# Optimization experiments

Measured on AMD Instinct MI355X. Metric: run time of the kernel, lower is better.

## Reference

```python
import jax, jax.numpy as jnp
import numpy as np
from jax import lax

B, T, C_IN = 64, 1000, 12
D_MODEL, D_STATE, D_CONV, EXPAND = 128, 16, 4, 2
D_INNER = EXPAND * D_MODEL          # 256
DT_RANK = (D_MODEL + 15) // 16      # ceil(d_model/16) = 8
NUM_CLASSES = 5


def setup_inputs() -> dict:
    key = jax.random.key(0)
    ks = jax.random.split(key, 12)
    s = 0.05
    f = jnp.float32
    return {
        "x": jax.random.normal(ks[0], (B, T, C_IN), f),
        # input projection Linear(C_IN, D_MODEL) with bias
        "ip_w": jax.random.normal(ks[1], (D_MODEL, C_IN), f) * s,
        "ip_b": jnp.zeros((D_MODEL,), f),
        # Mamba block params (mamba_ssm layout)
        "in_proj_w": jax.random.normal(ks[2], (2 * D_INNER, D_MODEL), f) * s,
        "conv_w": jax.random.normal(ks[3], (D_INNER, D_CONV), f) * s,
        "conv_b": jnp.zeros((D_INNER,), f),
        "x_proj_w": jax.random.normal(ks[4], (DT_RANK + 2 * D_STATE, D_INNER), f) * s,
        "dt_proj_w": jax.random.normal(ks[5], (D_INNER, DT_RANK), f) * s,
        "dt_proj_b": jax.random.uniform(ks[6], (D_INNER,), f, -4.0, -2.0),  # softplus -> small positive dt
        "A_log": jnp.log(jnp.tile(jnp.arange(1, D_STATE + 1, dtype=f), (D_INNER, 1))),
        "D_skip": jnp.ones((D_INNER,), f),
        "out_proj_w": jax.random.normal(ks[7], (D_MODEL, D_INNER), f) * s,
        # classifier head: Linear(128,64) -> ReLU -> Linear(64,5)
        "fc1_w": jax.random.normal(ks[8], (64, D_MODEL), f) * s,
        "fc1_b": jnp.zeros((64,), f),
        "fc2_w": jax.random.normal(ks[9], (NUM_CLASSES, 64), f) * s,
        "fc2_b": jnp.zeros((NUM_CLASSES,), f),
    }


def _silu(x):
    return x * jax.nn.sigmoid(x)


def _mamba(h, in_proj_w, conv_w, conv_b, x_proj_w, dt_proj_w, dt_proj_b,
           A_log, D_skip, out_proj_w):
    # h: (B, T, D_MODEL)
    xz = h @ in_proj_w.T                              # (B, T, 2*Di)
    xm, z = jnp.split(xz, 2, axis=-1)
    # depthwise causal conv over time (pad left d_conv-1)
    xp = jnp.pad(xm, ((0, 0), (D_CONV - 1, 0), (0, 0)))
    rhs = conv_w.T[:, None, :]                        # (d_conv, 1, Di)
    xc = lax.conv_general_dilated(
        xp, rhs, (1,), 'VALID',
        dimension_numbers=('NHC', 'HIO', 'NHC'),
        feature_group_count=D_INNER) + conv_b
    u = _silu(xc)                                     # (B, T, Di)
    dbc = u @ x_proj_w.T                              # (B, T, dt_rank + 2N)
    dt = dbc[..., :DT_RANK]
    Bm = dbc[..., DT_RANK:DT_RANK + D_STATE]          # (B, T, N)
    Cm = dbc[..., DT_RANK + D_STATE:]                 # (B, T, N)
    delta = jax.nn.softplus(dt @ dt_proj_w.T + dt_proj_b)  # (B, T, Di)
    A = -jnp.exp(A_log)                               # (Di, N)

    def step(hst, inp):
        d_t, b_t, c_t, u_t = inp                      # (B,Di),(B,N),(B,N),(B,Di)
        dA = jnp.exp(d_t[..., None] * A)              # (B, Di, N)
        hst = dA * hst + (d_t * u_t)[..., None] * b_t[:, None, :]
        y_t = jnp.einsum('bdn,bn->bd', hst, c_t)
        return hst, y_t

    h0 = jnp.zeros((h.shape[0], D_INNER, D_STATE), h.dtype)
    _, ys = lax.scan(step, h0, (delta.transpose(1, 0, 2), Bm.transpose(1, 0, 2),
                                Cm.transpose(1, 0, 2), u.transpose(1, 0, 2)))
    y = ys.transpose(1, 0, 2) + u * D_skip            # (B, T, Di)
    y = y * _silu(z)
    return y @ out_proj_w.T                           # (B, T, D_MODEL)


def reference(x, ip_w, ip_b, in_proj_w, conv_w, conv_b, x_proj_w, dt_proj_w,
              dt_proj_b, A_log, D_skip, out_proj_w, fc1_w, fc1_b, fc2_w, fc2_b):
    h = x @ ip_w.T + ip_b                             # (B, T, D_MODEL)
    y = _mamba(h, in_proj_w, conv_w, conv_b, x_proj_w, dt_proj_w, dt_proj_b,
               A_log, D_skip, out_proj_w)
    last = y[:, -1, :]                                # (B, D_MODEL)
    hid = jax.nn.relu(last @ fc1_w.T + fc1_b)
    return hid @ fc2_w.T + fc2_b                      # (B, NUM_CLASSES)
```

## Files before the change

kernel.cpp:

```cpp
#include <hip/hip_runtime.h>
#include <cstddef>

#define T_LEN 1000
#define B_SZ 64
#define C_IN_ 12
#define D_MODEL_ 128
#define D_INNER_ 256
#define D_STATE_ 16
#define DT_RANK_ 8
#define N_CLS 5
#define NCH 5

typedef __attribute__((ext_vector_type(8))) short bf16x8;
typedef __attribute__((ext_vector_type(8))) unsigned short u16x8;
typedef __attribute__((ext_vector_type(4))) float f32x4;

__device__ __forceinline__ float fast_exp2(float x) {
#if __has_builtin(__builtin_amdgcn_exp2f)
  return __builtin_amdgcn_exp2f(x);
#else
  float r; asm volatile("v_exp_f32 %0, %1" : "=v"(r) : "v"(x)); return r;
#endif
}
__device__ __forceinline__ float fast_log2(float x) {
#if __has_builtin(__builtin_amdgcn_logf)
  return __builtin_amdgcn_logf(x);
#else
  float r; asm volatile("v_log_f32 %0, %1" : "=v"(r) : "v"(x)); return r;
#endif
}
__device__ __forceinline__ float fast_rcp(float x) {
#if __has_builtin(__builtin_amdgcn_rcpf)
  return __builtin_amdgcn_rcpf(x);
#else
  float r; asm volatile("v_rcp_f32 %0, %1" : "=v"(r) : "v"(x)); return r;
#endif
}
__device__ __forceinline__ float silu_f(float x) {
  float den = 1.f + fast_exp2(-x * 1.4426950408889634f);
  return x * fast_rcp(den);
}
__device__ __forceinline__ float softplus_f(float x) {
  const float L = 1.4426950408889634f, iL = 0.6931471805599453f;
  float e = fast_exp2(-fabsf(x) * L);
  float l = fast_log2(1.f + e) * iL;
  return fmaxf(x, 0.f) + l;
}
__device__ __forceinline__ unsigned short f2bf(float f) {
  unsigned u = __builtin_bit_cast(unsigned, f);
  u = u + 0x7FFFu + ((u >> 16) & 1u);
  return (unsigned short)(u >> 16);
}
__device__ __forceinline__ float bf2f(unsigned short h) {
  unsigned u = ((unsigned)h) << 16;
  return __builtin_bit_cast(float, u);
}

__global__ __launch_bounds__(256) void k0_prep(
    const float* __restrict__ x, const float* __restrict__ ip_w,
    const float* __restrict__ ip_b, const float* __restrict__ in_proj_w,
    char* __restrict__ h_pk, char* __restrict__ w_pk)
{
  __shared__ unsigned short pk_s[8192];
  __shared__ unsigned short pkw_s[32768];
  const int tid = threadIdx.x;

  if (blockIdx.x == 16) {
    if (blockIdx.y != 0) return;
    const int n = tid;
    for (int k = 0; k < D_MODEL_; ++k) {
      unsigned short v = f2bf(in_proj_w[(size_t)n * D_MODEL_ + k]);
      int off = ((n >> 4) * 4 + (k >> 5)) * 512 + ((k & 31) >> 3) * 128
              + (n & 15) * 8 + (k & 7);
      pkw_s[off] = v;
    }
    __syncthreads();
    const float4* s4 = (const float4*)pkw_s;
    float4* dst = (float4*)w_pk;
#pragma unroll
    for (int q = 0; q < 16; ++q) dst[tid * 16 + q] = s4[tid * 16 + q];
    return;
  }

  const int tile4 = blockIdx.x;
  const int b = blockIdx.y;
  const int rl = tid & 63;
  const int kc = (tid >> 6) * 32;
  const int t = tile4 * 64 + rl;

  float xr[C_IN_] = {0.f, 0.f, 0.f, 0.f, 0.f, 0.f, 0.f, 0.f, 0.f, 0.f, 0.f, 0.f};
  const bool valid = (t < T_LEN);
  if (valid) {
    const float4* xp = (const float4*)(x + ((size_t)b * T_LEN + t) * C_IN_);
    float4 v0 = xp[0], v1 = xp[1], v2 = xp[2];
    xr[0] = v0.x; xr[1] = v0.y; xr[2] = v0.z;  xr[3] = v0.w;
    xr[4] = v1.x; xr[5] = v1.y; xr[6] = v1.z;  xr[7] = v1.w;
    xr[8] = v2.x; xr[9] = v2.y; xr[10] = v2.z; xr[11] = v2.w;
  }
  for (int kk = 0; kk < 32; ++kk) {
    const int k = kc + kk;
    unsigned short v = 0;
    if (valid) {
      float acc = ip_b[k];
      const float* wr = ip_w + k * C_IN_;
#pragma unroll
      for (int c = 0; c < C_IN_; ++c) acc += xr[c] * wr[c];
      v = f2bf(acc);
    }
    int off = (rl >> 4) * 2048 + (k >> 5) * 512 + ((k & 31) >> 3) * 128
            + (rl & 15) * 8 + (k & 7);
    pk_s[off] = v;
  }
  __syncthreads();
  const float4* s4 = (const float4*)pk_s;
  float4* dst = (float4*)(h_pk + (size_t)(b * 64 + tile4 * 4) * 4096);
#pragma unroll
  for (int q = 0; q < 4; ++q) dst[tid * 4 + q] = s4[tid * 4 + q];
}

__global__ __launch_bounds__(256) void k1_u(
    const char* __restrict__ h_pk, const char* __restrict__ w_pk,
    const float* __restrict__ conv_w, const float* __restrict__ conv_b,
    float* __restrict__ u_out)
{
  __shared__ float xm[67][260];

  const int tile = blockIdx.x;
  const int b    = blockIdx.y;
  const int t0   = tile * 64;
  const int tid  = threadIdx.x;
  const int w    = tid >> 6;
  const int l    = tid & 63;

  {
    const char* achunk = h_pk + (size_t)(b * 64 + tile * 4 + w) * 4096;
    bf16x8 a0 = *(const bf16x8*)(achunk + 0 * 1024 + l * 16);
    bf16x8 a1 = *(const bf16x8*)(achunk + 1 * 1024 + l * 16);
    bf16x8 a2 = *(const bf16x8*)(achunk + 2 * 1024 + l * 16);
    bf16x8 a3 = *(const bf16x8*)(achunk + 3 * 1024 + l * 16);

    const int row_l = w * 16 + (l >> 4) * 4;
#pragma unroll
    for (int nt = 0; nt < 16; ++nt) {
      const char* wb = w_pk + (size_t)nt * 4096 + l * 16;
      bf16x8 b0 = *(const bf16x8*)(wb + 0 * 1024);
      bf16x8 b1 = *(const bf16x8*)(wb + 1 * 1024);
      bf16x8 b2 = *(const bf16x8*)(wb + 2 * 1024);
      bf16x8 b3 = *(const bf16x8*)(wb + 3 * 1024);
      f32x4 acc = {0.f, 0.f, 0.f, 0.f};
      acc = __builtin_amdgcn_mfma_f32_16x16x32_bf16(a0, b0, acc, 0, 0, 0);
      acc = __builtin_amdgcn_mfma_f32_16x16x32_bf16(a1, b1, acc, 0, 0, 0);
      acc = __builtin_amdgcn_mfma_f32_16x16x32_bf16(a2, b2, acc, 0, 0, 0);
      acc = __builtin_amdgcn_mfma_f32_16x16x32_bf16(a3, b3, acc, 0, 0, 0);
      const int col = nt * 16 + (l & 15);
#pragma unroll
      for (int r = 0; r < 4; ++r)
        xm[3 + row_l + r][col] = acc[r];
    }
  }

  {
    const int n = tid;
    float hac[3] = {0.f, 0.f, 0.f};
    if (tile > 0) {
      const char* wrow = w_pk + (size_t)(n >> 4) * 4096 + (n & 15) * 16;
#pragma unroll
      for (int kt = 0; kt < 4; ++kt)
#pragma unroll
        for (int lg = 0; lg < 4; ++lg) {
          u16x8 wv = *(const u16x8*)(wrow + kt * 1024 + lg * 256);
#pragma unroll
          for (int r = 0; r < 3; ++r) {
            const int t = t0 - 3 + r;
            const char* hc = h_pk + (size_t)(b * 64 + (t >> 4)) * 4096;
            u16x8 hv = *(const u16x8*)(hc + kt * 1024 + lg * 256 + (t & 15) * 16);
#pragma unroll
            for (int j = 0; j < 8; ++j) hac[r] += bf2f(hv[j]) * bf2f(wv[j]);
          }
        }
    }
#pragma unroll
    for (int r = 0; r < 3; ++r) xm[r][n] = hac[r];
  }
  __syncthreads();

  {
    const int n = tid;
    const float4 cw = *(const float4*)&conv_w[n * 4];
    const float  cb = conv_b[n];
    float x0 = xm[0][n], x1 = xm[1][n], x2 = xm[2][n];
    for (int i = 0; i < 64; ++i) {
      const int t = t0 + i;
      float x3 = xm[3 + i][n];
      if (t < T_LEN) {
        float s = cb + x0 * cw.x + x1 * cw.y + x2 * cw.z + x3 * cw.w;
        u_out[(((size_t)b * T_LEN + t) << 8) + n] = silu_f(s);
      }
      x0 = x1; x1 = x2; x2 = x3;
    }
  }
}

__global__ __launch_bounds__(256) void k3_delta(
    const float* __restrict__ u, const float* __restrict__ x_proj_w,
    const float* __restrict__ dt_proj_w, const float* __restrict__ dt_proj_b,
    float* __restrict__ delta_T, float* __restrict__ du_T,
    float* __restrict__ pk_bm, float* __restrict__ u_last)
{
  __shared__ float4 xp4[24][65];
  __shared__ float dt_s[64][9];
  __shared__ float bm_s[64][17];

  const int row0 = blockIdx.x * 64;
  const int tid = threadIdx.x;

  for (int f = tid; f < 24 * 64; f += 256) {
    int c = f >> 6, k4 = f & 63;
    xp4[c][k4] = *(const float4*)&x_proj_w[(size_t)c * 256 + k4 * 4];
  }
  const float4 w0 = *(const float4*)&dt_proj_w[(size_t)tid * 8];
  const float4 w1 = *(const float4*)&dt_proj_w[(size_t)tid * 8 + 4];
  const float bias = dt_proj_b[tid];
  __syncthreads();

  {
    const int r2 = tid >> 3, cg = tid & 7;
    const int ra = 2 * r2;
    const float4* ua4 = (const float4*)(u + (size_t)(row0 + ra) * 256);
    const float4* ub4 = (const float4*)(u + (size_t)(row0 + ra + 1) * 256);
    float a0 = 0.f, a1 = 0.f, a2 = 0.f, b0 = 0.f, b1 = 0.f, b2 = 0.f;
    for (int k4 = 0; k4 < 64; ++k4) {
      float4 a = ua4[k4], bb = ub4[k4];
      float4 q0 = xp4[cg * 3 + 0][k4];
      float4 q1 = xp4[cg * 3 + 1][k4];
      float4 q2 = xp4[cg * 3 + 2][k4];
      a0 += a.x * q0.x + a.y * q0.y + a.z * q0.z + a.w * q0.w;
      a1 += a.x * q1.x + a.y * q1.y + a.z * q1.z + a.w * q1.w;
      a2 += a.x * q2.x + a.y * q2.y + a.z * q2.z + a.w * q2.w;
      b0 += bb.x * q0.x + bb.y * q0.y + bb.z * q0.z + bb.w * q0.w;
      b1 += bb.x * q1.x + bb.y * q1.y + bb.z * q1.z + bb.w * q1.w;
      b2 += bb.x * q2.x + bb.y * q2.y + bb.z * q2.z + bb.w * q2.w;
    }
    float va[2][3] = {{a0, a1, a2}, {b0, b1, b2}};
#pragma unroll
    for (int rr = 0; rr < 2; ++rr)
#pragma unroll
      for (int c = 0; c < 3; ++c) {
        int col = cg * 3 + c;
        int row = ra + rr;
        if (col < 8) dt_s[row][col] = va[rr][c];
        else bm_s[row][col - 8] = va[rr][c];
      }
  }
  __syncthreads();

  for (int g = 0; g < 8; ++g) {
    float dd[8], uu[8];
#pragma unroll
    for (int j = 0; j < 8; ++j) {
      int r = g * 8 + j;
      float pre = bias
        + dt_s[r][0] * w0.x + dt_s[r][1] * w0.y + dt_s[r][2] * w0.z + dt_s[r][3] * w0.w
        + dt_s[r][4] * w1.x + dt_s[r][5] * w1.y + dt_s[r][6] * w1.z + dt_s[r][7] * w1.w;
      float dlt = softplus_f(pre);
      size_t o = (size_t)(row0 + r) * 256 + tid;
      float uv = u[o];
      dd[j] = dlt;
      uu[j] = dlt * uv;
      int rowg = row0 + r;
      if ((rowg - (rowg / 1000) * 1000) == 999)
        u_last[(rowg / 1000) * 256 + tid] = uv;
    }
    int row = row0 + g * 8;
    int bb_ = row / 1000;
    int t   = row - bb_ * 1000;
    size_t rb = ((size_t)(bb_ * 256 + tid)) * 1000 + t;
    *(float4*)&delta_T[rb]     = make_float4(dd[0], dd[1], dd[2], dd[3]);
    *(float4*)&delta_T[rb + 4] = make_float4(dd[4], dd[5], dd[6], dd[7]);
    *(float4*)&du_T[rb]        = make_float4(uu[0], uu[1], uu[2], uu[3]);
    *(float4*)&du_T[rb + 4]    = make_float4(uu[4], uu[5], uu[6], uu[7]);
  }
  if (tid < 16) {
    for (int g = 0; g < 8; ++g) {
      float pb[8];
#pragma unroll
      for (int j = 0; j < 8; ++j) pb[j] = bm_s[g * 8 + j][tid];
      int row = row0 + g * 8;
      int bb_ = row / 1000;
      int t   = row - bb_ * 1000;
      size_t base = (((size_t)bb_ * 250 + (t >> 2)) * 16 + tid) * 4;
      *(float4*)&pk_bm[base]      = make_float4(pb[0], pb[1], pb[2], pb[3]);
      *(float4*)&pk_bm[base + 64] = make_float4(pb[4], pb[5], pb[6], pb[7]);
    }
  }
}

__global__ __launch_bounds__(256) void k4_scan(
    const float* __restrict__ delta_T, const float* __restrict__ du_T,
    const float* __restrict__ pk_bm, const float* __restrict__ A_log,
    float* __restrict__ Qb, float* __restrict__ Pb)
{
  __shared__ float bs[50][16][4];

  const int d0 = blockIdx.x * 16;
  const int b  = blockIdx.y;
  const int c  = blockIdx.z;
  const int tid = threadIdx.x;
  const int dl = tid >> 4;
  const int n  = tid & 15;
  const int d  = d0 + dl;

  {
    const float4* src = (const float4*)(pk_bm + ((size_t)b * 250 + (size_t)c * 50) * 64);
    float4* dst = (float4*)bs;
    for (int f = tid; f < 800; f += 256) dst[f] = src[f];
  }
  const float A2 = -expf(A_log[(size_t)d * 16 + n]) * 1.4426950408889634f;
  const float* dp = delta_T + ((size_t)(b * 256 + d)) * 1000 + c * 200;
  const float* xp = du_T    + ((size_t)(b * 256 + d)) * 1000 + c * 200;
  __syncthreads();

  float s = 0.f, sum = 0.f;
#pragma unroll
  for (int i = 0; i < 50; ++i) {
    float4 dv = *(const float4*)(dp + 4 * i);
    float4 xv = *(const float4*)(xp + 4 * i);
    float4 bv = *(const float4*)&bs[i][n][0];
    sum += (dv.x + dv.y) + (dv.z + dv.w);
    s = fast_exp2(dv.x * A2) * s + xv.x * bv.x;
    s = fast_exp2(dv.y * A2) * s + xv.y * bv.y;
    s = fast_exp2(dv.z * A2) * s + xv.z * bv.z;
    s = fast_exp2(dv.w * A2) * s + xv.w * bv.w;
  }

  const size_t o = (size_t)c * 262144 + (size_t)b * 4096 + (size_t)d0 * 16 + tid;
  Qb[o] = s;
  Pb[o] = fast_exp2(A2 * sum);
}

__global__ __launch_bounds__(256) void k4b_combine(
    const float* __restrict__ Qb, const float* __restrict__ Pb,
    float* __restrict__ state_out)
{
  const size_t g = (size_t)blockIdx.x * 256 + threadIdx.x;
  float s = Qb[g];
#pragma unroll
  for (int c = 1; c < NCH; ++c)
    s = Qb[(size_t)c * 262144 + g] + Pb[(size_t)c * 262144 + g] * s;
  state_out[g] = s;
}

__global__ __launch_bounds__(256) void k5_head(
    const float* __restrict__ x, const float* __restrict__ ip_w,
    const float* __restrict__ ip_b, const float* __restrict__ in_proj_w,
    const float* __restrict__ x_proj_w, const float* __restrict__ u_last,
    const float* __restrict__ state, const float* __restrict__ D_skip,
    const float* __restrict__ out_proj_w, const float* __restrict__ fc1_w,
    const float* __restrict__ fc1_b, const float* __restrict__ fc2_w,
    const float* __restrict__ fc2_b, float* __restrict__ out)
{
  const int b = blockIdx.x, tid = threadIdx.x;
  __shared__ float hl[128], ul[256], zs[256], cm[16], yv[256], ov[128], hid[64];
  if (tid < 128) {
    float acc = ip_b[tid];
    const float* xr = x + ((size_t)b * T_LEN + (T_LEN - 1)) * C_IN_;
#pragma unroll
    for (int c = 0; c < C_IN_; ++c) acc += xr[c] * ip_w[tid * C_IN_ + c];
    hl[tid] = acc;
  }
  ul[tid] = u_last[b * 256 + tid];
  __syncthreads();
  {
    float acc = 0.f;
    const float4* wv = (const float4*)(in_proj_w + (size_t)(256 + tid) * 128);
    const float4* h4 = (const float4*)hl;
    for (int k = 0; k < 32; ++k) {
      float4 a = wv[k], c = h4[k];
      acc += c.x * a.x + c.y * a.y + c.z * a.z + c.w * a.w;
    }
    zs[tid] = silu_f(acc);
  }
  if (tid < 16) {
    float acc = 0.f;
    const float4* wv = (const float4*)(x_proj_w + (size_t)(24 + tid) * 256);
    const float4* u4 = (const float4*)ul;
    for (int k = 0; k < 64; ++k) {
      float4 a = wv[k], c = u4[k];
      acc += c.x * a.x + c.y * a.y + c.z * a.z + c.w * a.w;
    }
    cm[tid] = acc;
  }
  __syncthreads();
  {
    const float* st = state + ((size_t)b * 256 + tid) * 16;
    float acc = 0.f;
#pragma unroll
    for (int n = 0; n < 16; ++n) acc += st[n] * cm[n];
    yv[tid] = (acc + ul[tid] * D_skip[tid]) * zs[tid];
  }
  __syncthreads();
  if (tid < 128) {
    float acc = 0.f;
    const float4* wv = (const float4*)(out_proj_w + (size_t)tid * 256);
    const float4* y4 = (const float4*)yv;
    for (int k = 0; k < 64; ++k) {
      float4 a = wv[k], c = y4[k];
      acc += c.x * a.x + c.y * a.y + c.z * a.z + c.w * a.w;
    }
    ov[tid] = acc;
  }
  __syncthreads();
  if (tid < 64) {
    float acc = fc1_b[tid];
    const float4* wv = (const float4*)(fc1_w + (size_t)tid * 128);
    const float4* o4 = (const float4*)ov;
    for (int k = 0; k < 32; ++k) {
      float4 a = wv[k], c = o4[k];
      acc += c.x * a.x + c.y * a.y + c.z * a.z + c.w * a.w;
    }
    hid[tid] = fmaxf(acc, 0.f);
  }
  __syncthreads();
  if (tid < N_CLS) {
    float acc = fc2_b[tid];
    const float* wv = fc2_w + (size_t)tid * 64;
    for (int k = 0; k < 64; ++k) acc += hid[k] * wv[k];
    out[b * N_CLS + tid] = acc;
  }
}

extern "C" void kernel_launch(void* const* d_in, const int* in_sizes, int n_in,
                              void* d_out, int out_size, void* d_ws, size_t ws_size,
                              hipStream_t stream) {
  (void)in_sizes; (void)n_in; (void)out_size; (void)ws_size;
  const float* x         = (const float*)d_in[0];
  const float* ip_w      = (const float*)d_in[1];
  const float* ip_b      = (const float*)d_in[2];
  const float* in_proj_w = (const float*)d_in[3];
  const float* conv_w    = (const float*)d_in[4];
  const float* conv_b    = (const float*)d_in[5];
  const float* x_proj_w  = (const float*)d_in[6];
  const float* dt_proj_w = (const float*)d_in[7];
  const float* dt_proj_b = (const float*)d_in[8];
  const float* A_log     = (const float*)d_in[9];
  const float* D_skip    = (const float*)d_in[10];
  const float* out_proj_w= (const float*)d_in[11];
  const float* fc1_w     = (const float*)d_in[12];
  const float* fc1_b     = (const float*)d_in[13];
  const float* fc2_w     = (const float*)d_in[14];
  const float* fc2_b     = (const float*)d_in[15];
  float* out = (float*)d_out;

  float* u       = (float*)d_ws;
  float* delta_T = u + (size_t)16384000;
  float* du_T    = delta_T + (size_t)16384000;
  float* pk_bm   = du_T + (size_t)16384000;
  float* state   = pk_bm + (size_t)1024000;
  float* u_last  = state + (size_t)262144;
  char* h_pk = (char*)delta_T;
  char* w_pk = h_pk + (size_t)64 * 64 * 4096;
  float* Qb  = u;
  float* Pb  = u + (size_t)2000000;

  k0_prep<<<dim3(17, 64), 256, 0, stream>>>(x, ip_w, ip_b, in_proj_w, h_pk, w_pk);
  k1_u<<<dim3(16, 64), 256, 0, stream>>>(h_pk, w_pk, conv_w, conv_b, u);
  k3_delta<<<1000, 256, 0, stream>>>(u, x_proj_w, dt_proj_w, dt_proj_b,
                                     delta_T, du_T, pk_bm, u_last);
  k4_scan<<<dim3(16, 64, NCH), 256, 0, stream>>>(delta_T, du_T, pk_bm, A_log, Qb, Pb);
  k4b_combine<<<1024, 256, 0, stream>>>(Qb, Pb, state);
  k5_head<<<64, 256, 0, stream>>>(x, ip_w, ip_b, in_proj_w, x_proj_w, u_last, state,
                                  D_skip, out_proj_w, fc1_w, fc1_b, fc2_w, fc2_b, out);
}
```

Before: 218.2 us.

## Transpose delta/du stores through LDS and double scan time chunks

The delta kernel now stages its 16-row tiles of delta and delta*u in shared memory (reusing the x_proj weight buffer) so each thread writes coalesced float4 runs along time for 4 channels, instead of per-channel 8-element strided writes. The chunked scan splits time into 10 chunks of 100 steps instead of 5 of 200, which doubles the grid and halves the serial dependency chain per thread. The cost is extra barriers and LDS traffic in the delta kernel, and twice as many partial states for the combine kernel to read. The Pb offset is moved so the larger partial buffers do not overlap.

```diff
diff --git a/kernel.cpp b/kernel.cpp
--- a/kernel.cpp
+++ b/kernel.cpp
@@ -9,7 +9,8 @@
 #define D_STATE_ 16
 #define DT_RANK_ 8
 #define N_CLS 5
-#define NCH 5
+#define NCH 10
+#define CT4 25
 
 typedef __attribute__((ext_vector_type(8))) short bf16x8;
 typedef __attribute__((ext_vector_type(8))) unsigned short u16x8;
@@ -207,7 +208,9 @@
     float* __restrict__ delta_T, float* __restrict__ du_T,
     float* __restrict__ pk_bm, float* __restrict__ u_last)
 {
-  __shared__ float4 xp4[24][65];
+  __shared__ __align__(16) float smem[24 * 65 * 4];
+  float4 (*xp4)[65] = reinterpret_cast<float4(*)[65]>(smem);
+  float* tx = smem;
   __shared__ float dt_s[64][9];
   __shared__ float bm_s[64][17];
 
@@ -254,11 +257,11 @@
   }
   __syncthreads();
 
-  for (int g = 0; g < 8; ++g) {
-    float dd[8], uu[8];
-#pragma unroll
-    for (int j = 0; j < 8; ++j) {
-      int r = g * 8 + j;
+  for (int c16 = 0; c16 < 4; ++c16) {
+    float dd[16], uu[16];
+#pragma unroll
+    for (int j = 0; j < 16; ++j) {
+      int r = c16 * 16 + j;
       float pre = bias
         + dt_s[r][0] * w0.x + dt_s[r][1] * w0.y + dt_s[r][2] * w0.z + dt_s[r][3] * w0.w
         + dt_s[r][4] * w1.x + dt_s[r][5] * w1.y + dt_s[r][6] * w1.z + dt_s[r][7] * w1.w;
@@ -271,14 +274,36 @@
       if ((rowg - (rowg / 1000) * 1000) == 999)
         u_last[(rowg / 1000) * 256 + tid] = uv;
     }
-    int row = row0 + g * 8;
-    int bb_ = row / 1000;
-    int t   = row - bb_ * 1000;
-    size_t rb = ((size_t)(bb_ * 256 + tid)) * 1000 + t;
-    *(float4*)&delta_T[rb]     = make_float4(dd[0], dd[1], dd[2], dd[3]);
-    *(float4*)&delta_T[rb + 4] = make_float4(dd[4], dd[5], dd[6], dd[7]);
-    *(float4*)&du_T[rb]        = make_float4(uu[0], uu[1], uu[2], uu[3]);
-    *(float4*)&du_T[rb + 4]    = make_float4(uu[4], uu[5], uu[6], uu[7]);
+#pragma unroll
+    for (int j = 0; j < 16; ++j) tx[tid * 17 + j] = dd[j];
+    __syncthreads();
+#pragma unroll
+    for (int q = 0; q < 4; ++q) {
+      int d_ = (tid >> 2) + 64 * q;
+      int t4 = (tid & 3) * 4;
+      float4 v = make_float4(tx[d_ * 17 + t4], tx[d_ * 17 + t4 + 1],
+                             tx[d_ * 17 + t4 + 2], tx[d_ * 17 + t4 + 3]);
+      int rowg = row0 + c16 * 16 + t4;
+      int bb = rowg / 1000;
+      int t = rowg - bb * 1000;
+      *(float4*)&delta_T[((size_t)(bb * 256 + d_)) * 1000 + t] = v;
+    }
+    __syncthreads();
+#pragma unroll
+    for (int j = 0; j < 16; ++j) tx[tid * 17 + j] = uu[j];
+    __syncthreads();
+#pragma unroll
+    for (int q = 0; q < 4; ++q) {
+      int d_ = (tid >> 2) + 64 * q;
+      int t4 = (tid & 3) * 4;
+      float4 v = make_float4(tx[d_ * 17 + t4], tx[d_ * 17 + t4 + 1],
+                             tx[d_ * 17 + t4 + 2], tx[d_ * 17 + t4 + 3]);
+      int rowg = row0 + c16 * 16 + t4;
+      int bb = rowg / 1000;
+      int t = rowg - bb * 1000;
+      *(float4*)&du_T[((size_t)(bb * 256 + d_)) * 1000 + t] = v;
+    }
+    __syncthreads();
   }
   if (tid < 16) {
     for (int g = 0; g < 8; ++g) {
@@ -300,7 +325,7 @@
     const float* __restrict__ pk_bm, const float* __restrict__ A_log,
     float* __restrict__ Qb, float* __restrict__ Pb)
 {
-  __shared__ float bs[50][16][4];
+  __shared__ float bs[CT4][16][4];
 
   const int d0 = blockIdx.x * 16;
   const int b  = blockIdx.y;
@@ -311,18 +336,18 @@
   const int d  = d0 + dl;
 
   {
-    const float4* src = (const float4*)(pk_bm + ((size_t)b * 250 + (size_t)c * 50) * 64);
+    const float4* src = (const float4*)(pk_bm + ((size_t)b * 250 + (size_t)c * CT4) * 64);
     float4* dst = (float4*)bs;
-    for (int f = tid; f < 800; f += 256) dst[f] = src[f];
+    for (int f = tid; f < CT4 * 16; f += 256) dst[f] = src[f];
   }
   const float A2 = -expf(A_log[(size_t)d * 16 + n]) * 1.4426950408889634f;
-  const float* dp = delta_T + ((size_t)(b * 256 + d)) * 1000 + c * 200;
-  const float* xp = du_T    + ((size_t)(b * 256 + d)) * 1000 + c * 200;
+  const float* dp = delta_T + ((size_t)(b * 256 + d)) * 1000 + c * 100;
+  const float* xp = du_T    + ((size_t)(b * 256 + d)) * 1000 + c * 100;
   __syncthreads();
 
   float s = 0.f, sum = 0.f;
 #pragma unroll
-  for (int i = 0; i < 50; ++i) {
+  for (int i = 0; i < CT4; ++i) {
     float4 dv = *(const float4*)(dp + 4 * i);
     float4 xv = *(const float4*)(xp + 4 * i);
     float4 bv = *(const float4*)&bs[i][n][0];
@@ -460,7 +485,7 @@
   char* h_pk = (char*)delta_T;
   char* w_pk = h_pk + (size_t)64 * 64 * 4096;
   float* Qb  = u;
-  float* Pb  = u + (size_t)2000000;
+  float* Pb  = u + (size_t)4000000;
 
   k0_prep<<<dim3(17, 64), 256, 0, stream>>>(x, ip_w, ip_b, in_proj_w, h_pk, w_pk);
   k1_u<<<dim3(16, 64), 256, 0, stream>>>(h_pk, w_pk, conv_w, conv_b, u);
```

Result: faster. 209.7 us (-3.9%).
